# Optimization experiments

Measured on AMD Instinct MI355X. Metric: run time of the kernel, lower is better.

The kernel has to match this reference:

```python
import jax, jax.numpy as jnp
import numpy as np

N, T, H, D = 8, 192, 1024, 128
P = 4            # t_patch_size (kernel = stride)
TP = T // P      # 48 patch tokens
E = 16384
HOUR, WDAY = 48, 7


def conv1d_patch(e, W, b):
    # e: [B, Cin, T]; W: [Cout, Cin, P]; kernel == stride == P (non-overlapping)
    B, Ci, Tt = e.shape
    e = e.reshape(B, Ci, Tt // P, P)
    return jnp.einsum('bctk,ock->bot', e, W) + b[None, :, None]  # [B, Cout, T']


def gcn_propagate(x, src, dst, coef):
    # x: [B, H, D] ; symmetric-normalized sparse A_hat @ x
    msg = x[:, src, :] * coef[None, :, None]
    return jnp.zeros_like(x).at[:, dst, :].add(msg)


def setup_inputs() -> dict:
    key = jax.random.key(0)
    ks = jax.random.split(key, 12)
    x = jax.random.normal(ks[0], (N, 1, T, H, 1), dtype=jnp.float32)
    x_mark = jax.random.randint(ks[1], (N, T, 2), 0, 7).astype(jnp.int64)
    edges = jax.random.randint(ks[2], (E, 2), 0, H).astype(jnp.int64)
    node_split = jnp.arange(H, dtype=jnp.int64).reshape(4, 256)
    s = 0.02
    params = {
        'hour_emb': jax.random.normal(ks[3], (HOUR, D), jnp.float32) * s,
        'weekday_emb': jax.random.normal(ks[4], (WDAY, D), jnp.float32) * s,
        'timeconv_w': jax.random.normal(ks[5], (D, D, P), jnp.float32) * s,
        'timeconv_b': jnp.zeros((D,), jnp.float32),
        'tconv_w': jax.random.normal(ks[6], (D, 1, P), jnp.float32) * s,
        'tconv_b': jnp.zeros((D,), jnp.float32),
        'W1': jax.random.normal(ks[7], (D, D), jnp.float32) * s,
        'b1': jnp.zeros((D,), jnp.float32),
        'W2': jax.random.normal(ks[8], (D, D), jnp.float32) * s,
        'b2': jnp.zeros((D,), jnp.float32),
    }
    return dict(x=x, x_mark=x_mark, edges=edges, node_split=node_split, **params)


def reference(x, x_mark, edges, node_split, hour_emb, weekday_emb,
              timeconv_w, timeconv_b, tconv_w, tconv_b, W1, b1, W2, b2):
    # ---- TimeEmb (TemporalEmbedding, hour_num='48') ----
    hour_x = hour_emb[x_mark[:, :, 1]]        # [N, T, D]
    wday_x = weekday_emb[x_mark[:, :, 0]]     # [N, T, D]
    time_emb = conv1d_patch((hour_x + wday_x).transpose(0, 2, 1),
                            timeconv_w, timeconv_b).transpose(0, 2, 1)  # [N, T', D]

    # ---- temporal value embedding ----
    xv = jnp.squeeze(x, (1, 4)).transpose(0, 2, 1).reshape(N * H, 1, T)  # [N*H,1,T]
    tv = conv1d_patch(xv, tconv_w, tconv_b)                 # [N*H, D, T']
    tv = tv.transpose(0, 2, 1).reshape(N, H, TP, D)         # [N, H, T', D]
    tv = tv.transpose(0, 2, 1, 3).reshape(N * TP, H, D)     # [N*T', H, D]

    # ---- 2-layer GCN with self-loops + symmetric normalization ----
    src = jnp.concatenate([edges[:, 0], jnp.arange(H)])
    dst = jnp.concatenate([edges[:, 1], jnp.arange(H)])
    deg = jnp.zeros((H,), tv.dtype).at[dst].add(1.0)
    coef = jax.lax.rsqrt(deg[src] * deg[dst])
    h = jax.nn.relu(gcn_propagate(tv, src, dst, coef) @ W1 + b1)
    token = gcn_propagate(h, src, dst, coef) @ W2 + b2      # [N*T', H, D]
    token = token.reshape(N, TP, H, D)

    # ---- per-group gather + mean pooling, interleaved per time step ----
    G = node_split.shape[0]
    grouped = token[:, :, node_split.reshape(-1), :].reshape(N, TP, G, -1, D)
    token = grouped.mean(axis=3).reshape(N, TP * G, D)      # [N, T'*G, D]

    time_rep = jnp.repeat(time_emb, G, axis=1)              # [N, T'*G, D]
    out = token + time_rep  # is_time == 1; eval mode -> no dropout
    return out, time_rep
```

## Files before the change

### kernel.cpp

```cpp
#include <hip/hip_runtime.h>
#include <hip/hip_bf16.h>

#define NN 8
#define TT 192
#define HH 1024
#define DD 128
#define TPP 48
#define EE 16384
#define NEDGE (EE + HH)
#define BB (NN * TPP)
#define NOUT (NN * TT * DD)

typedef short bf16x8 __attribute__((ext_vector_type(8)));
typedef float f32x4 __attribute__((ext_vector_type(4)));

__device__ __forceinline__ float us2f(unsigned short u) {
  union { unsigned i; float f; } t;
  t.i = ((unsigned)u) << 16;
  return t.f;
}

__device__ __forceinline__ void acc6(float cf, unsigned u0, unsigned u1, unsigned u2,
                                     float& a0, float& a1, float& a2, float& a3,
                                     float& a4, float& a5) {
  union { unsigned i; float f; } lo, hi;
  lo.i = u0 << 16; hi.i = u0 & 0xffff0000u;
  a0 = fmaf(cf, lo.f, a0); a1 = fmaf(cf, hi.f, a1);
  lo.i = u1 << 16; hi.i = u1 & 0xffff0000u;
  a2 = fmaf(cf, lo.f, a2); a3 = fmaf(cf, hi.f, a3);
  lo.i = u2 << 16; hi.i = u2 & 0xffff0000u;
  a4 = fmaf(cf, lo.f, a4); a5 = fmaf(cf, hi.f, a5);
}

__global__ __launch_bounds__(256) void k_setup(
    const int* __restrict__ edges, int* __restrict__ degE,
    const int* __restrict__ node_split, int* __restrict__ inv,
    const float* __restrict__ tw, float* __restrict__ twT,
    float* __restrict__ zbuf,
    const float* __restrict__ x, __hip_bfloat16* __restrict__ Xall,
    const float* __restrict__ tcw, const float* __restrict__ tcb,
    const float* __restrict__ W1, float* __restrict__ CW,
    const float* __restrict__ W2, __hip_bfloat16* __restrict__ w2sw) {
  __shared__ float tile[64][65];
  int tid = threadIdx.x, bid = blockIdx.x;
  if (bid < 384) {
    int i = bid * 256 + tid;
    if (i < EE) atomicAdd(&degE[edges[2 * i + 1]], 1);
    if (i < HH) inv[node_split[i]] = i;
    if (i < 65536) twT[(i & 511) * DD + (i >> 9)] = tw[i];
    if (i < 6144) zbuf[i] = 0.f;

    int tt = bid % 24, st = bid / 24;
    int t0 = tt * 64, s0 = st * 64;
    int sl = tid & 63, r4 = tid >> 6;
#pragma unroll 4
    for (int ii = 0; ii < 16; ++ii) {
      int tl = ii * 4 + r4;
      tile[tl][sl] = x[(size_t)(t0 + tl) * HH + s0 + sl];
    }
    __syncthreads();
#pragma unroll 4
    for (int ii = 0; ii < 16; ++ii) {
      int sl2 = ii * 4 + r4;
      Xall[(size_t)(s0 + sl2) * 1536 + t0 + sl] = __float2bfloat16(tile[sl][sl2]);
    }
  } else {
    int ex = (bid - 384) * 256 + tid;
    if (ex < 640) {
      int j = ex >> 7, o = ex & 127;
      float acc = 0.f;
      if (j < 4)
        for (int d = 0; d < DD; ++d) acc = fmaf(tcw[d * 4 + j], W1[d * DD + o], acc);
      else
        for (int d = 0; d < DD; ++d) acc = fmaf(tcb[d], W1[d * DD + o], acc);
      CW[j * DD + o] = acc;
    }
    int ew = ex - 1024;
    if (ew >= 0 && ew < 16384) {
      int n = ew >> 7, k = ew & 127;
      int dstb = n * 256 + (((k >> 3) ^ (n & 7)) * 16) + (k & 7) * 2;
      w2sw[dstb >> 1] = __float2bfloat16(W2[k * DD + n]);
    }
  }
}

__global__ __launch_bounds__(256) void k_scatter(
    const int* __restrict__ edges, const int* __restrict__ degE,
    const int* __restrict__ inv, int* __restrict__ fill,
    int* __restrict__ csr_src, float* __restrict__ csr_coef,
    float* __restrict__ csum, float* __restrict__ QT, int* __restrict__ row_ptr) {
  __shared__ int rp[1024];
  __shared__ int wsumS[4];
  int tid = threadIdx.x, lane = tid & 63, wid = tid >> 6;
  int4 d4 = ((const int4*)degE)[tid];
  int l0 = d4.x + 1, l1 = d4.y + 1, l2 = d4.z + 1, l3 = d4.w + 1;
  int lsum = l0 + l1 + l2 + l3;
  int incl = lsum;
#pragma unroll
  for (int off = 1; off < 64; off <<= 1) {
    int u = __shfl_up(incl, off, 64);
    if (lane >= off) incl += u;
  }
  if (lane == 63) wsumS[wid] = incl;
  __syncthreads();
  int base = 0;
  if (wid > 0) base += wsumS[0];
  if (wid > 1) base += wsumS[1];
  if (wid > 2) base += wsumS[2];
  int excl = base + incl - lsum;
  rp[4 * tid] = excl;
  rp[4 * tid + 1] = excl + l0;
  rp[4 * tid + 2] = excl + l0 + l1;
  rp[4 * tid + 3] = excl + l0 + l1 + l2;
  __syncthreads();
  if (blockIdx.x == 0) {
    for (int i = tid; i < 1024; i += 256) row_ptr[i] = rp[i];
    if (tid == 0) row_ptr[1024] = NEDGE;
  }
  int e = blockIdx.x * 256 + tid;
  if (e < NEDGE) {
    int s, dt;
    if (e < EE) { s = edges[2 * e]; dt = edges[2 * e + 1]; }
    else        { s = dt = e - EE; }
    float ds = (float)(degE[s] + 1);
    float dd = (float)(degE[dt] + 1);
    float cf = rsqrtf(ds * dd);
    int pos = atomicAdd(&fill[dt], 1);
    int at = rp[dt] + pos;
    csr_src[at] = s;
    csr_coef[at] = cf;
    atomicAdd(&csum[dt], cf);
    int g = inv[dt] >> 8;
    atomicAdd(&QT[s * 4 + g], cf * (1.0f / 256.0f));
  }
}

__global__ __launch_bounds__(256) void k_spmm(
    const int* __restrict__ row_ptr, const int* __restrict__ csr_src,
    const float* __restrict__ csr_coef, const __hip_bfloat16* __restrict__ Xall,
    __hip_bfloat16* __restrict__ xbar,
    const int* __restrict__ xm, const float* __restrict__ hour_emb,
    const float* __restrict__ wday_emb, const float* __restrict__ twT,
    const float* __restrict__ tcb, float* __restrict__ out) {
  __shared__ float sL[2][512];
  __shared__ int sS[256];
  __shared__ float sC[256];
  int tid = threadIdx.x, bid = blockIdx.x;
  if (bid < HH) {
    int h = bid;
    int j0 = row_ptr[h], j1 = row_ptr[h + 1];
    int cnt = j1 - j0;
    int cs = cnt < 256 ? cnt : 256;
    if (tid < cs) { sS[tid] = csr_src[j0 + tid]; sC[tid] = csr_coef[j0 + tid]; }
    __syncthreads();
    float a0 = 0.f, a1 = 0.f, a2 = 0.f, a3 = 0.f, a4 = 0.f, a5 = 0.f;
    int j = 0;
    for (; j + 4 <= cs; j += 4) {
      const unsigned* x0 = (const unsigned*)(Xall + (size_t)sS[j] * 1536);
      const unsigned* x1 = (const unsigned*)(Xall + (size_t)sS[j + 1] * 1536);
      const unsigned* x2 = (const unsigned*)(Xall + (size_t)sS[j + 2] * 1536);
      const unsigned* x3 = (const unsigned*)(Xall + (size_t)sS[j + 3] * 1536);
      unsigned u00 = x0[tid], u01 = x0[tid + 256], u02 = x0[tid + 512];
      unsigned u10 = x1[tid], u11 = x1[tid + 256], u12 = x1[tid + 512];
      unsigned u20 = x2[tid], u21 = x2[tid + 256], u22 = x2[tid + 512];
      unsigned u30 = x3[tid], u31 = x3[tid + 256], u32 = x3[tid + 512];
      float c0 = sC[j], c1 = sC[j + 1], c2 = sC[j + 2], c3 = sC[j + 3];
      acc6(c0, u00, u01, u02, a0, a1, a2, a3, a4, a5);
      acc6(c1, u10, u11, u12, a0, a1, a2, a3, a4, a5);
      acc6(c2, u20, u21, u22, a0, a1, a2, a3, a4, a5);
      acc6(c3, u30, u31, u32, a0, a1, a2, a3, a4, a5);
    }
    for (; j < cs; ++j) {
      const unsigned* xr = (const unsigned*)(Xall + (size_t)sS[j] * 1536);
      unsigned u0 = xr[tid], u1 = xr[tid + 256], u2 = xr[tid + 512];
      acc6(sC[j], u0, u1, u2, a0, a1, a2, a3, a4, a5);
    }
    for (; j < cnt; ++j) {
      int s = csr_src[j0 + j];
      float cf = csr_coef[j0 + j];
      const unsigned* xr = (const unsigned*)(Xall + (size_t)s * 1536);
      unsigned u0 = xr[tid], u1 = xr[tid + 256], u2 = xr[tid + 512];
      acc6(cf, u0, u1, u2, a0, a1, a2, a3, a4, a5);
    }
    unsigned* xw = (unsigned*)(xbar + (size_t)h * 1536);
    union { __hip_bfloat16 h2[2]; unsigned u; } pk;
    pk.h2[0] = __float2bfloat16(a0); pk.h2[1] = __float2bfloat16(a1);
    xw[tid] = pk.u;
    pk.h2[0] = __float2bfloat16(a2); pk.h2[1] = __float2bfloat16(a3);
    xw[tid + 256] = pk.u;
    pk.h2[0] = __float2bfloat16(a4); pk.h2[1] = __float2bfloat16(a5);
    xw[tid + 512] = pk.u;
  } else {
    int bb = bid - HH;
    int half = tid >> 7, o = tid & 127;
    int b = bb * 2 + half;
    int n = b / TPP, tp = b % TPP;
    for (int k = 0; k < 4; ++k) {
      int t = tp * 4 + k;
      int wd = xm[(n * TT + t) * 2 + 0];
      int hr = xm[(n * TT + t) * 2 + 1];
      sL[half][o * 4 + k] = hour_emb[hr * DD + o] + wday_emb[wd * DD + o];
    }
    __syncthreads();
    float a0 = tcb[o], a1 = 0.f, a2 = 0.f, a3 = 0.f;
    for (int j = 0; j < 512; j += 4) {
      a0 = fmaf(sL[half][j + 0], twT[(j + 0) * DD + o], a0);
      a1 = fmaf(sL[half][j + 1], twT[(j + 1) * DD + o], a1);
      a2 = fmaf(sL[half][j + 2], twT[(j + 2) * DD + o], a2);
      a3 = fmaf(sL[half][j + 3], twT[(j + 3) * DD + o], a3);
    }
    float acc = (a0 + a1) + (a2 + a3);
    size_t base = (size_t)NOUT + ((size_t)n * TT + tp * 4) * DD + o;
    out[base] = acc;
    out[base + DD] = acc;
    out[base + 2 * DD] = acc;
    out[base + 3 * DD] = acc;
  }
}

__global__ __launch_bounds__(128) void k_red(const __hip_bfloat16* __restrict__ xbar,
                                             const float* __restrict__ csum,
                                             const float* __restrict__ QT,
                                             const float* __restrict__ CW,
                                             const float* __restrict__ b1,
                                             float* __restrict__ ypar) {
  __shared__ float4 xb4[256];
  __shared__ float4 qv[256];
  __shared__ float csv[256];
  __shared__ float yL[512];
  int tid = threadIdx.x, bid = blockIdx.x;
  int b = bid >> 2, qt = bid & 3;
  for (int r = tid; r < 256; r += 128) {
    int h = qt * 256 + r;
    ushort4 us = *(const ushort4*)(xbar + (size_t)h * 1536 + b * 4);
    xb4[r] = make_float4(us2f(us.x), us2f(us.y), us2f(us.z), us2f(us.w));
    qv[r] = *(const float4*)(QT + h * 4);
    csv[r] = csum[h];
  }
  int lane = tid & 63, w = tid >> 6;
  int o0 = lane, o1 = lane + 64;
  float cw0a = CW[o0], cw1a = CW[DD + o0], cw2a = CW[2 * DD + o0];
  float cw3a = CW[3 * DD + o0], cw4a = CW[4 * DD + o0];
  float cw0b = CW[o1], cw1b = CW[DD + o1], cw2b = CW[2 * DD + o1];
  float cw3b = CW[3 * DD + o1], cw4b = CW[4 * DD + o1];
  float b1a = b1[o0], b1b = b1[o1];
  __syncthreads();
  float y0a = 0.f, y1a = 0.f, y2a = 0.f, y3a = 0.f;
  float y0b = 0.f, y1b = 0.f, y2b = 0.f, y3b = 0.f;
  int h0 = w * 128;
#pragma unroll 4
  for (int hh = h0; hh < h0 + 128; ++hh) {
    float4 xv = xb4[hh];
    float4 q = qv[hh];
    float c = csv[hh];
    float t0 = fmaf(c, cw4a, b1a);
    t0 = fmaf(xv.x, cw0a, t0);
    t0 = fmaf(xv.y, cw1a, t0);
    t0 = fmaf(xv.z, cw2a, t0);
    t0 = fmaf(xv.w, cw3a, t0);
    t0 = fmaxf(t0, 0.f);
    float t1 = fmaf(c, cw4b, b1b);
    t1 = fmaf(xv.x, cw0b, t1);
    t1 = fmaf(xv.y, cw1b, t1);
    t1 = fmaf(xv.z, cw2b, t1);
    t1 = fmaf(xv.w, cw3b, t1);
    t1 = fmaxf(t1, 0.f);
    y0a = fmaf(q.x, t0, y0a); y1a = fmaf(q.y, t0, y1a);
    y2a = fmaf(q.z, t0, y2a); y3a = fmaf(q.w, t0, y3a);
    y0b = fmaf(q.x, t1, y0b); y1b = fmaf(q.y, t1, y1b);
    y2b = fmaf(q.z, t1, y2b); y3b = fmaf(q.w, t1, y3b);
  }
  if (w == 0) {
    yL[o0] = y0a; yL[128 + o0] = y1a; yL[256 + o0] = y2a; yL[384 + o0] = y3a;
    yL[o1] = y0b; yL[128 + o1] = y1b; yL[256 + o1] = y2b; yL[384 + o1] = y3b;
  }
  __syncthreads();
  if (w == 1) {
    yL[o0] += y0a; yL[128 + o0] += y1a; yL[256 + o0] += y2a; yL[384 + o0] += y3a;
    yL[o1] += y0b; yL[128 + o1] += y1b; yL[256 + o1] += y2b; yL[384 + o1] += y3b;
  }
  __syncthreads();
  float* yp = ypar + ((size_t)qt * BB + b) * 512;
  for (int i = tid; i < 512; i += 128) yp[i] = yL[i];
}

__global__ __launch_bounds__(256, 2) void k_out(const float* __restrict__ ypar,
                                                const __hip_bfloat16* __restrict__ w2sw,
                                                const float* __restrict__ b2,
                                                float* __restrict__ out) {
  __shared__ __align__(16) char Wr[32768];
  __shared__ __align__(16) char Gr[16384];
  int tid = threadIdx.x;
  int m0 = blockIdx.x * 64;
  {
    const uint4* ws = (const uint4*)w2sw;
    uint4* wd = (uint4*)Wr;
    for (int i = tid; i < 2048; i += 256) wd[i] = ws[i];
  }
#pragma unroll 4
  for (int it = 0; it < 16; ++it) {
    int pi = it * 256 + tid;
    int row = pi >> 6, kp = pi & 63;
    int base = (m0 + row) * 128 + 2 * kp;
    float s0 = 0.f, s1 = 0.f;
#pragma unroll
    for (int p = 0; p < 4; ++p) {
      s0 += ypar[(size_t)p * (BB * 512) + base];
      s1 += ypar[(size_t)p * (BB * 512) + base + 1];
    }
    union { __hip_bfloat16 h[2]; unsigned u; } pk;
    pk.h[0] = __float2bfloat16(s0);
    pk.h[1] = __float2bfloat16(s1);
    *(unsigned*)(Gr + row * 256 + (((kp >> 2) ^ (row & 7)) * 16) + (kp & 3) * 4) = pk.u;
  }
  int lane = tid & 63, w = tid >> 6;
  int colq = lane & 15, quad = lane >> 4;
  float bo[8];
#pragma unroll
  for (int jn = 0; jn < 8; ++jn) bo[jn] = b2[jn * 16 + colq];
  __syncthreads();

  f32x4 acc[8];
#pragma unroll
  for (int jn = 0; jn < 8; ++jn) acc[jn] = (f32x4){0.f, 0.f, 0.f, 0.f};
  int arow = w * 16 + colq;
#pragma unroll
  for (int kc = 0; kc < 4; ++kc) {
    bf16x8 af = *(const bf16x8*)(Gr + arow * 256 + (((kc * 4 + quad) ^ (arow & 7)) * 16));
#pragma unroll
    for (int jn = 0; jn < 8; ++jn) {
      int nr = jn * 16 + colq;
      bf16x8 bf = *(const bf16x8*)(Wr + nr * 256 + (((kc * 4 + quad) ^ (nr & 7)) * 16));
      acc[jn] = __builtin_amdgcn_mfma_f32_16x16x32_bf16(af, bf, acc[jn], 0, 0, 0);
    }
  }
#pragma unroll
  for (int reg = 0; reg < 4; ++reg) {
    int m = m0 + w * 16 + quad * 4 + reg;
    int b = m >> 2, g = m & 3;
    int n_ = b / TPP, tp = b % TPP;
    size_t rb = ((size_t)(n_ * TT + tp * 4 + g)) * DD;
#pragma unroll
    for (int jn = 0; jn < 8; ++jn) {
      int o = jn * 16 + colq;
      out[rb + o] = acc[jn][reg] + bo[jn] + out[(size_t)NOUT + rb + o];
    }
  }
}

extern "C" void kernel_launch(void* const* d_in, const int* in_sizes, int n_in,
                              void* d_out, int out_size, void* d_ws, size_t ws_size,
                              hipStream_t stream) {
  const float* x = (const float*)d_in[0];
  const int* xm = (const int*)d_in[1];
  const int* edges = (const int*)d_in[2];
  const int* node_split = (const int*)d_in[3];
  const float* hour_emb = (const float*)d_in[4];
  const float* wday_emb = (const float*)d_in[5];
  const float* timeconv_w = (const float*)d_in[6];
  const float* timeconv_b = (const float*)d_in[7];
  const float* tcw = (const float*)d_in[8];
  const float* tcb = (const float*)d_in[9];
  const float* W1 = (const float*)d_in[10];
  const float* b1 = (const float*)d_in[11];
  const float* W2 = (const float*)d_in[12];
  const float* b2 = (const float*)d_in[13];
  float* out = (float*)d_out;

  char* w = (char*)d_ws;
  int* degE = (int*)(w + 0);
  int* fill = (int*)(w + 4096);
  float* csum = (float*)(w + 8192);
  float* QT = (float*)(w + 12288);
  int* row_ptr = (int*)(w + 28672);
  int* inv = (int*)(w + 33024);
  int* csr_src = (int*)(w + 37120);
  float* csr_coef = (float*)(w + 106752);
  __hip_bfloat16* w2sw = (__hip_bfloat16*)(w + 176384);
  float* CW = (float*)(w + 209152);
  float* twT = (float*)(w + 213248);
  __hip_bfloat16* Xall = (__hip_bfloat16*)(w + 475392);
  float* ypar = (float*)(w + 475392);
  __hip_bfloat16* xbar = (__hip_bfloat16*)(w + 3621120);

  hipMemsetAsync(degE, 0, 4096, stream);
  k_setup<<<452, 256, 0, stream>>>(edges, degE, node_split, inv, timeconv_w, twT,
                                   (float*)(w + 4096), x, Xall, tcw, tcb, W1, CW, W2,
                                   w2sw);
  k_scatter<<<68, 256, 0, stream>>>(edges, degE, inv, fill, csr_src, csr_coef, csum,
                                    QT, row_ptr);
  k_spmm<<<HH + BB / 2, 256, 0, stream>>>(row_ptr, csr_src, csr_coef, Xall, xbar, xm,
                                          hour_emb, wday_emb, twT, timeconv_b, out);
  k_red<<<BB * 4, 128, 0, stream>>>(xbar, csum, QT, CW, b1, ypar);
  k_out<<<24, 256, 0, stream>>>(ypar, w2sw, b2, out);
}
```

Baseline: 143.7 us.

## Fuse degree histogram and CSR scatter into setup kernel, drop scatter launch

Removes the separate k_scatter launch by having 68 extra blocks in k_setup each build the full degree histogram in shared memory from all edges, compute the prefix sum locally, and scatter their slice of edges into CSR. The time-embedding conv blocks move from k_spmm into k_setup and read the conv weight in its original layout, so the twT transpose is gone. This cuts one kernel launch and the global degree atomics. In exchange, every scatter block redundantly reads all 16K edges and does shared-memory atomics, and the time-conv weight reads become per-thread strided rather than coalesced.

```diff
diff --git a/kernel.cpp b/kernel.cpp
--- a/kernel.cpp
+++ b/kernel.cpp
@@ -33,23 +33,23 @@
 }
 
 __global__ __launch_bounds__(256) void k_setup(
-    const int* __restrict__ edges, int* __restrict__ degE,
-    const int* __restrict__ node_split, int* __restrict__ inv,
-    const float* __restrict__ tw, float* __restrict__ twT,
-    float* __restrict__ zbuf,
+    const int* __restrict__ edges, const int* __restrict__ node_split,
     const float* __restrict__ x, __hip_bfloat16* __restrict__ Xall,
     const float* __restrict__ tcw, const float* __restrict__ tcb,
     const float* __restrict__ W1, float* __restrict__ CW,
-    const float* __restrict__ W2, __hip_bfloat16* __restrict__ w2sw) {
+    const float* __restrict__ W2, __hip_bfloat16* __restrict__ w2sw,
+    int* __restrict__ fill, int* __restrict__ csr_src, float* __restrict__ csr_coef,
+    float* __restrict__ csum, float* __restrict__ QT, int* __restrict__ row_ptr,
+    const int* __restrict__ xm, const float* __restrict__ hour_emb,
+    const float* __restrict__ wday_emb, const float* __restrict__ tw,
+    float* __restrict__ out) {
   __shared__ float tile[64][65];
+  __shared__ int hist[1024];
+  __shared__ int rp2[1024];
+  __shared__ int invS[1024];
+  __shared__ int wsumS[4];
   int tid = threadIdx.x, bid = blockIdx.x;
   if (bid < 384) {
-    int i = bid * 256 + tid;
-    if (i < EE) atomicAdd(&degE[edges[2 * i + 1]], 1);
-    if (i < HH) inv[node_split[i]] = i;
-    if (i < 65536) twT[(i & 511) * DD + (i >> 9)] = tw[i];
-    if (i < 6144) zbuf[i] = 0.f;
-
     int tt = bid % 24, st = bid / 24;
     int t0 = tt * 64, s0 = st * 64;
     int sl = tid & 63, r4 = tid >> 6;
@@ -64,7 +64,7 @@
       int sl2 = ii * 4 + r4;
       Xall[(size_t)(s0 + sl2) * 1536 + t0 + sl] = __float2bfloat16(tile[sl][sl2]);
     }
-  } else {
+  } else if (bid < 452) {
     int ex = (bid - 384) * 256 + tid;
     if (ex < 640) {
       int j = ex >> 7, o = ex & 127;
@@ -81,117 +81,57 @@
       int dstb = n * 256 + (((k >> 3) ^ (n & 7)) * 16) + (k & 7) * 2;
       w2sw[dstb >> 1] = __float2bfloat16(W2[k * DD + n]);
     }
-  }
-}
-
-__global__ __launch_bounds__(256) void k_scatter(
-    const int* __restrict__ edges, const int* __restrict__ degE,
-    const int* __restrict__ inv, int* __restrict__ fill,
-    int* __restrict__ csr_src, float* __restrict__ csr_coef,
-    float* __restrict__ csum, float* __restrict__ QT, int* __restrict__ row_ptr) {
-  __shared__ int rp[1024];
-  __shared__ int wsumS[4];
-  int tid = threadIdx.x, lane = tid & 63, wid = tid >> 6;
-  int4 d4 = ((const int4*)degE)[tid];
-  int l0 = d4.x + 1, l1 = d4.y + 1, l2 = d4.z + 1, l3 = d4.w + 1;
-  int lsum = l0 + l1 + l2 + l3;
-  int incl = lsum;
-#pragma unroll
-  for (int off = 1; off < 64; off <<= 1) {
-    int u = __shfl_up(incl, off, 64);
-    if (lane >= off) incl += u;
-  }
-  if (lane == 63) wsumS[wid] = incl;
-  __syncthreads();
-  int base = 0;
-  if (wid > 0) base += wsumS[0];
-  if (wid > 1) base += wsumS[1];
-  if (wid > 2) base += wsumS[2];
-  int excl = base + incl - lsum;
-  rp[4 * tid] = excl;
-  rp[4 * tid + 1] = excl + l0;
-  rp[4 * tid + 2] = excl + l0 + l1;
-  rp[4 * tid + 3] = excl + l0 + l1 + l2;
-  __syncthreads();
-  if (blockIdx.x == 0) {
-    for (int i = tid; i < 1024; i += 256) row_ptr[i] = rp[i];
-    if (tid == 0) row_ptr[1024] = NEDGE;
-  }
-  int e = blockIdx.x * 256 + tid;
-  if (e < NEDGE) {
+  } else if (bid < 520) {
+    int lane = tid & 63, wid = tid >> 6;
+    for (int i = tid; i < 1024; i += 256) hist[i] = 1;
+    for (int i = tid; i < 1024; i += 256) invS[node_split[i]] = i;
+    __syncthreads();
+    for (int e = tid; e < EE; e += 256) atomicAdd(&hist[edges[2 * e + 1]], 1);
+    __syncthreads();
+    int4 d4 = ((const int4*)hist)[tid];
+    int l0 = d4.x, l1 = d4.y, l2 = d4.z, l3 = d4.w;
+    int lsum = l0 + l1 + l2 + l3;
+    int incl = lsum;
+#pragma unroll
+    for (int off = 1; off < 64; off <<= 1) {
+      int u = __shfl_up(incl, off, 64);
+      if (lane >= off) incl += u;
+    }
+    if (lane == 63) wsumS[wid] = incl;
+    __syncthreads();
+    int base = 0;
+    if (wid > 0) base += wsumS[0];
+    if (wid > 1) base += wsumS[1];
+    if (wid > 2) base += wsumS[2];
+    int excl = base + incl - lsum;
+    rp2[4 * tid] = excl;
+    rp2[4 * tid + 1] = excl + l0;
+    rp2[4 * tid + 2] = excl + l0 + l1;
+    rp2[4 * tid + 3] = excl + l0 + l1 + l2;
+    __syncthreads();
+    if (bid == 452) {
+      for (int i = tid; i < 1024; i += 256) row_ptr[i] = rp2[i];
+      if (tid == 0) row_ptr[1024] = NEDGE;
+    }
+    int e = (bid - 452) * 256 + tid;
     int s, dt;
-    if (e < EE) { s = edges[2 * e]; dt = edges[2 * e + 1]; }
-    else        { s = dt = e - EE; }
-    float ds = (float)(degE[s] + 1);
-    float dd = (float)(degE[dt] + 1);
-    float cf = rsqrtf(ds * dd);
+    if (e < EE) {
+      int2 ed = ((const int2*)edges)[e];
+      s = ed.x; dt = ed.y;
+    } else {
+      s = dt = e - EE;
+    }
+    float cf = rsqrtf((float)hist[s] * (float)hist[dt]);
     int pos = atomicAdd(&fill[dt], 1);
-    int at = rp[dt] + pos;
+    int at = rp2[dt] + pos;
     csr_src[at] = s;
     csr_coef[at] = cf;
     atomicAdd(&csum[dt], cf);
-    int g = inv[dt] >> 8;
+    int g = invS[dt] >> 8;
     atomicAdd(&QT[s * 4 + g], cf * (1.0f / 256.0f));
-  }
-}
-
-__global__ __launch_bounds__(256) void k_spmm(
-    const int* __restrict__ row_ptr, const int* __restrict__ csr_src,
-    const float* __restrict__ csr_coef, const __hip_bfloat16* __restrict__ Xall,
-    __hip_bfloat16* __restrict__ xbar,
-    const int* __restrict__ xm, const float* __restrict__ hour_emb,
-    const float* __restrict__ wday_emb, const float* __restrict__ twT,
-    const float* __restrict__ tcb, float* __restrict__ out) {
-  __shared__ float sL[2][512];
-  __shared__ int sS[256];
-  __shared__ float sC[256];
-  int tid = threadIdx.x, bid = blockIdx.x;
-  if (bid < HH) {
-    int h = bid;
-    int j0 = row_ptr[h], j1 = row_ptr[h + 1];
-    int cnt = j1 - j0;
-    int cs = cnt < 256 ? cnt : 256;
-    if (tid < cs) { sS[tid] = csr_src[j0 + tid]; sC[tid] = csr_coef[j0 + tid]; }
-    __syncthreads();
-    float a0 = 0.f, a1 = 0.f, a2 = 0.f, a3 = 0.f, a4 = 0.f, a5 = 0.f;
-    int j = 0;
-    for (; j + 4 <= cs; j += 4) {
-      const unsigned* x0 = (const unsigned*)(Xall + (size_t)sS[j] * 1536);
-      const unsigned* x1 = (const unsigned*)(Xall + (size_t)sS[j + 1] * 1536);
-      const unsigned* x2 = (const unsigned*)(Xall + (size_t)sS[j + 2] * 1536);
-      const unsigned* x3 = (const unsigned*)(Xall + (size_t)sS[j + 3] * 1536);
-      unsigned u00 = x0[tid], u01 = x0[tid + 256], u02 = x0[tid + 512];
-      unsigned u10 = x1[tid], u11 = x1[tid + 256], u12 = x1[tid + 512];
-      unsigned u20 = x2[tid], u21 = x2[tid + 256], u22 = x2[tid + 512];
-      unsigned u30 = x3[tid], u31 = x3[tid + 256], u32 = x3[tid + 512];
-      float c0 = sC[j], c1 = sC[j + 1], c2 = sC[j + 2], c3 = sC[j + 3];
-      acc6(c0, u00, u01, u02, a0, a1, a2, a3, a4, a5);
-      acc6(c1, u10, u11, u12, a0, a1, a2, a3, a4, a5);
-      acc6(c2, u20, u21, u22, a0, a1, a2, a3, a4, a5);
-      acc6(c3, u30, u31, u32, a0, a1, a2, a3, a4, a5);
-    }
-    for (; j < cs; ++j) {
-      const unsigned* xr = (const unsigned*)(Xall + (size_t)sS[j] * 1536);
-      unsigned u0 = xr[tid], u1 = xr[tid + 256], u2 = xr[tid + 512];
-      acc6(sC[j], u0, u1, u2, a0, a1, a2, a3, a4, a5);
-    }
-    for (; j < cnt; ++j) {
-      int s = csr_src[j0 + j];
-      float cf = csr_coef[j0 + j];
-      const unsigned* xr = (const unsigned*)(Xall + (size_t)s * 1536);
-      unsigned u0 = xr[tid], u1 = xr[tid + 256], u2 = xr[tid + 512];
-      acc6(cf, u0, u1, u2, a0, a1, a2, a3, a4, a5);
-    }
-    unsigned* xw = (unsigned*)(xbar + (size_t)h * 1536);
-    union { __hip_bfloat16 h2[2]; unsigned u; } pk;
-    pk.h2[0] = __float2bfloat16(a0); pk.h2[1] = __float2bfloat16(a1);
-    xw[tid] = pk.u;
-    pk.h2[0] = __float2bfloat16(a2); pk.h2[1] = __float2bfloat16(a3);
-    xw[tid + 256] = pk.u;
-    pk.h2[0] = __float2bfloat16(a4); pk.h2[1] = __float2bfloat16(a5);
-    xw[tid + 512] = pk.u;
   } else {
-    int bb = bid - HH;
+    __shared__ float sL[2][512];
+    int bb = bid - 520;
     int half = tid >> 7, o = tid & 127;
     int b = bb * 2 + half;
     int n = b / TPP, tp = b % TPP;
@@ -202,12 +142,13 @@
       sL[half][o * 4 + k] = hour_emb[hr * DD + o] + wday_emb[wd * DD + o];
     }
     __syncthreads();
+    const float* twr = tw + (size_t)o * 512;
     float a0 = tcb[o], a1 = 0.f, a2 = 0.f, a3 = 0.f;
     for (int j = 0; j < 512; j += 4) {
-      a0 = fmaf(sL[half][j + 0], twT[(j + 0) * DD + o], a0);
-      a1 = fmaf(sL[half][j + 1], twT[(j + 1) * DD + o], a1);
-      a2 = fmaf(sL[half][j + 2], twT[(j + 2) * DD + o], a2);
-      a3 = fmaf(sL[half][j + 3], twT[(j + 3) * DD + o], a3);
+      a0 = fmaf(sL[half][j + 0], twr[j + 0], a0);
+      a1 = fmaf(sL[half][j + 1], twr[j + 1], a1);
+      a2 = fmaf(sL[half][j + 2], twr[j + 2], a2);
+      a3 = fmaf(sL[half][j + 3], twr[j + 3], a3);
     }
     float acc = (a0 + a1) + (a2 + a3);
     size_t base = (size_t)NOUT + ((size_t)n * TT + tp * 4) * DD + o;
@@ -216,6 +157,57 @@
     out[base + 2 * DD] = acc;
     out[base + 3 * DD] = acc;
   }
+}
+
+__global__ __launch_bounds__(256) void k_spmm(
+    const int* __restrict__ row_ptr, const int* __restrict__ csr_src,
+    const float* __restrict__ csr_coef, const __hip_bfloat16* __restrict__ Xall,
+    __hip_bfloat16* __restrict__ xbar) {
+  __shared__ int sS[256];
+  __shared__ float sC[256];
+  int tid = threadIdx.x, h = blockIdx.x;
+  int j0 = row_ptr[h], j1 = row_ptr[h + 1];
+  int cnt = j1 - j0;
+  int cs = cnt < 256 ? cnt : 256;
+  if (tid < cs) { sS[tid] = csr_src[j0 + tid]; sC[tid] = csr_coef[j0 + tid]; }
+  __syncthreads();
+  float a0 = 0.f, a1 = 0.f, a2 = 0.f, a3 = 0.f, a4 = 0.f, a5 = 0.f;
+  int j = 0;
+  for (; j + 4 <= cs; j += 4) {
+    const unsigned* x0 = (const unsigned*)(Xall + (size_t)sS[j] * 1536);
+    const unsigned* x1 = (const unsigned*)(Xall + (size_t)sS[j + 1] * 1536);
+    const unsigned* x2 = (const unsigned*)(Xall + (size_t)sS[j + 2] * 1536);
+    const unsigned* x3 = (const unsigned*)(Xall + (size_t)sS[j + 3] * 1536);
+    unsigned u00 = x0[tid], u01 = x0[tid + 256], u02 = x0[tid + 512];
+    unsigned u10 = x1[tid], u11 = x1[tid + 256], u12 = x1[tid + 512];
+    unsigned u20 = x2[tid], u21 = x2[tid + 256], u22 = x2[tid + 512];
+    unsigned u30 = x3[tid], u31 = x3[tid + 256], u32 = x3[tid + 512];
+    float c0 = sC[j], c1 = sC[j + 1], c2 = sC[j + 2], c3 = sC[j + 3];
+    acc6(c0, u00, u01, u02, a0, a1, a2, a3, a4, a5);
+    acc6(c1, u10, u11, u12, a0, a1, a2, a3, a4, a5);
+    acc6(c2, u20, u21, u22, a0, a1, a2, a3, a4, a5);
+    acc6(c3, u30, u31, u32, a0, a1, a2, a3, a4, a5);
+  }
+  for (; j < cs; ++j) {
+    const unsigned* xr = (const unsigned*)(Xall + (size_t)sS[j] * 1536);
+    unsigned u0 = xr[tid], u1 = xr[tid + 256], u2 = xr[tid + 512];
+    acc6(sC[j], u0, u1, u2, a0, a1, a2, a3, a4, a5);
+  }
+  for (; j < cnt; ++j) {
+    int s = csr_src[j0 + j];
+    float cf = csr_coef[j0 + j];
+    const unsigned* xr = (const unsigned*)(Xall + (size_t)s * 1536);
+    unsigned u0 = xr[tid], u1 = xr[tid + 256], u2 = xr[tid + 512];
+    acc6(cf, u0, u1, u2, a0, a1, a2, a3, a4, a5);
+  }
+  unsigned* xw = (unsigned*)(xbar + (size_t)h * 1536);
+  union { __hip_bfloat16 h2[2]; unsigned u; } pk;
+  pk.h2[0] = __float2bfloat16(a0); pk.h2[1] = __float2bfloat16(a1);
+  xw[tid] = pk.u;
+  pk.h2[0] = __float2bfloat16(a2); pk.h2[1] = __float2bfloat16(a3);
+  xw[tid + 256] = pk.u;
+  pk.h2[0] = __float2bfloat16(a4); pk.h2[1] = __float2bfloat16(a5);
+  xw[tid + 512] = pk.u;
 }
 
 __global__ __launch_bounds__(128) void k_red(const __hip_bfloat16* __restrict__ xbar,
@@ -368,29 +360,23 @@
   float* out = (float*)d_out;
 
   char* w = (char*)d_ws;
-  int* degE = (int*)(w + 0);
   int* fill = (int*)(w + 4096);
   float* csum = (float*)(w + 8192);
   float* QT = (float*)(w + 12288);
   int* row_ptr = (int*)(w + 28672);
-  int* inv = (int*)(w + 33024);
   int* csr_src = (int*)(w + 37120);
   float* csr_coef = (float*)(w + 106752);
   __hip_bfloat16* w2sw = (__hip_bfloat16*)(w + 176384);
   float* CW = (float*)(w + 209152);
-  float* twT = (float*)(w + 213248);
   __hip_bfloat16* Xall = (__hip_bfloat16*)(w + 475392);
   float* ypar = (float*)(w + 475392);
   __hip_bfloat16* xbar = (__hip_bfloat16*)(w + 3621120);
 
-  hipMemsetAsync(degE, 0, 4096, stream);
-  k_setup<<<452, 256, 0, stream>>>(edges, degE, node_split, inv, timeconv_w, twT,
-                                   (float*)(w + 4096), x, Xall, tcw, tcb, W1, CW, W2,
-                                   w2sw);
-  k_scatter<<<68, 256, 0, stream>>>(edges, degE, inv, fill, csr_src, csr_coef, csum,
-                                    QT, row_ptr);
-  k_spmm<<<HH + BB / 2, 256, 0, stream>>>(row_ptr, csr_src, csr_coef, Xall, xbar, xm,
-                                          hour_emb, wday_emb, twT, timeconv_b, out);
+  hipMemsetAsync(w + 4096, 0, 24576, stream);
+  k_setup<<<712, 256, 0, stream>>>(edges, node_split, x, Xall, tcw, tcb, W1, CW, W2,
+                                   w2sw, fill, csr_src, csr_coef, csum, QT, row_ptr,
+                                   xm, hour_emb, wday_emb, timeconv_w, out);
+  k_spmm<<<HH, 256, 0, stream>>>(row_ptr, csr_src, csr_coef, Xall, xbar);
   k_red<<<BB * 4, 128, 0, stream>>>(xbar, csum, QT, CW, b1, ypar);
   k_out<<<24, 256, 0, stream>>>(ypar, w2sw, b2, out);
 }
```

New measurement: 141.3 us. No clear change (-1.7%).
